# Kernel optimization log

Measured on AMD Instinct MI355X. Metric: run time of the kernel, lower is better.

## Reference

```python
import jax, jax.numpy as jnp
import numpy as np

EPS = 1e-5

def setup_inputs() -> dict:
    key = jax.random.key(0)
    ks = jax.random.split(key, 12)
    B = 4096
    x = jax.random.normal(ks[0], (B, 28, 28, 1), dtype=jnp.float32)
    # BatchNorm1d(1) affine params (applied per-channel over active sites)
    bn_gamma = jnp.ones((1,), jnp.float32)
    bn_beta = jnp.zeros((1,), jnp.float32)
    # SubMConv2d weights, HWIO layout
    w1 = jax.random.normal(ks[1], (3, 3, 1, 32), jnp.float32) * 0.1
    b1 = jax.random.normal(ks[2], (32,), jnp.float32) * 0.01
    w2 = jax.random.normal(ks[3], (3, 3, 32, 64), jnp.float32) * 0.05
    b2 = jax.random.normal(ks[4], (64,), jnp.float32) * 0.01
    # FC layers (torch Linear: y = x @ W.T + b)
    fcw1 = jax.random.normal(ks[5], (128, 14 * 14 * 64), jnp.float32) * 0.01
    fcb1 = jnp.zeros((128,), jnp.float32)
    fcw2 = jax.random.normal(ks[6], (10, 128), jnp.float32) * 0.05
    fcb2 = jnp.zeros((10,), jnp.float32)
    return {"x": x, "bn_gamma": bn_gamma, "bn_beta": bn_beta,
            "w1": w1, "b1": b1, "w2": w2, "b2": b2,
            "fcw1": fcw1, "fcb1": fcb1, "fcw2": fcw2, "fcb2": fcb2}

def _subm_conv(feat, mask, w, b):
    # Submanifold conv: inactive inputs are zero (already masked), and the
    # output coordinate set equals the input active set -> mask the output.
    y = jax.lax.conv_general_dilated(
        feat, w, window_strides=(1, 1), padding='SAME',
        dimension_numbers=('NHWC', 'HWIO', 'NHWC'))
    return jnp.where(mask, y + b, 0.0)

def reference(x, bn_gamma, bn_beta, w1, b1, w2, b2, fcw1, fcb1, fcw2, fcb2):
    # from_dense: active sites are locations with nonzero feature. [B,28,28,1]
    mask = (x != 0)  # single channel -> site mask [B,28,28,1]
    maskf = mask.astype(x.dtype)
    # BatchNorm1d(1) on the [N_active, 1] sparse feature tensor (batch stats)
    n = jnp.maximum(maskf.sum(), 1.0)
    mean = (x * maskf).sum() / n
    var = (jnp.square(x - mean) * maskf).sum() / n
    feat = maskf * (bn_gamma * (x - mean) * jax.lax.rsqrt(var + EPS) + bn_beta)
    # SubMConv2d(1,32,3,1) + ReLU
    h = jax.nn.relu(_subm_conv(feat, mask, w1, b1))  # [B,28,28,32]
    # SubMConv2d(32,64,3,1) + ReLU
    h = jax.nn.relu(_subm_conv(h, mask, w2, b2))     # [B,28,28,64]
    # SparseMaxPool2d(2,2): max over active sites per window; since values are
    # post-ReLU (>=0) and inactive sites hold 0, dense maxpool is exact, and
    # fully-inactive windows correctly yield 0 after ToDense.
    h = jax.lax.reduce_window(h, -jnp.inf, jax.lax.max,
                              (1, 2, 2, 1), (1, 2, 2, 1), 'VALID')  # [B,14,14,64]
    # ToDense gives NCHW [B,64,14,14]; torch.flatten uses C-major order
    h = jnp.transpose(h, (0, 3, 1, 2)).reshape(h.shape[0], -1)  # [B,12544]
    # dropout1/dropout2 are identity in eval mode
    h = jax.nn.relu(h @ fcw1.T + fcb1)
    logits = h @ fcw2.T + fcb2
    return jax.nn.log_softmax(logits, axis=1)
```

## Files before the change

kernel.cpp:

```cpp
#include <hip/hip_runtime.h>
#include <stdint.h>

typedef unsigned short u16;
typedef unsigned int u32;
typedef __attribute__((ext_vector_type(8))) short bf16x8;
typedef __attribute__((ext_vector_type(4))) float f32x4;

__device__ __forceinline__ u16 f2bf(float f) {
    u32 u = __float_as_uint(f);
    u32 r = (u + 0x7fffu + ((u >> 16) & 1u)) >> 16;
    return (u16)r;
}

__device__ __forceinline__ void gload16(const u16* src, u16* dst) {
    __builtin_amdgcn_global_load_lds(
        (const __attribute__((address_space(1))) u32*)src,
        (__attribute__((address_space(3))) u32*)dst, 16, 0, 0);
}

__global__ __launch_bounds__(256) void k_stats(const float* __restrict__ x, int n,
                                               float* __restrict__ stats) {
    int t = blockIdx.x * 256 + threadIdx.x;
    int stride = gridDim.x * 256;
    float c = 0.f, s = 0.f, ss = 0.f;
    for (int i = t; i < n; i += stride) {
        float v = x[i];
        if (v != 0.f) { c += 1.f; s += v; ss = fmaf(v, v, ss); }
    }
    for (int off = 32; off > 0; off >>= 1) {
        c  += __shfl_down(c, off);
        s  += __shfl_down(s, off);
        ss += __shfl_down(ss, off);
    }
    __shared__ float red[3][4];
    int lane = threadIdx.x & 63, wv = threadIdx.x >> 6;
    if (lane == 0) { red[0][wv] = c; red[1][wv] = s; red[2][wv] = ss; }
    __syncthreads();
    if (threadIdx.x == 0) {
        atomicAdd(&stats[0], red[0][0] + red[0][1] + red[0][2] + red[0][3]);
        atomicAdd(&stats[1], red[1][0] + red[1][1] + red[1][2] + red[1][3]);
        atomicAdd(&stats[2], red[2][0] + red[2][1] + red[2][2] + red[2][3]);
    }
}

__global__ void k_finalize(const float* __restrict__ g, const float* __restrict__ b,
                           float* __restrict__ stats) {
    float n = stats[0]; if (n < 1.f) n = 1.f;
    float mean = stats[1] / n;
    float var = stats[2] / n - mean * mean;
    if (var < 0.f) var = 0.f;
    float scale = g[0] * rsqrtf(var + 1e-5f);
    stats[4] = scale;
    stats[5] = b[0] - mean * scale;
}

__global__ __launch_bounds__(256) void k_prep(const float* __restrict__ w2,
                                              u16* __restrict__ w2b) {
    int i = blockIdx.x * 256 + threadIdx.x;
    if (i < 9 * 64 * 32) {
        int tap = i >> 11, rem = i & 2047, co = rem >> 5, ci = rem & 31;
        w2b[i] = f2bf(w2[tap * 2048 + ci * 64 + co]);
    }
}

__global__ __launch_bounds__(256) void k_prepw(const float* __restrict__ fcw1,
                                               u16* __restrict__ fcw1b, int n) {
    int i = blockIdx.x * 256 + threadIdx.x;
    if (i < n) fcw1b[i] = f2bf(fcw1[i]);
}

__global__ __launch_bounds__(256, 2) void k_conv(const float* __restrict__ x,
    const float* __restrict__ w1, const float* __restrict__ b1,
    const u16* __restrict__ w2b, const float* __restrict__ b2,
    const float* __restrict__ stats, u16* __restrict__ pooled)
{
    __shared__ u16 h1[28800];
    __shared__ float feat[30][30];
    __shared__ unsigned char mk[784];
    const int t = threadIdx.x;
    const int b = blockIdx.x;
    const int lane = t & 63;
    const int wv = t >> 6;
    const int lg = lane >> 4;
    const int lr = lane & 15;

    bf16x8 wf[9][4];
    #pragma unroll
    for (int tap = 0; tap < 9; ++tap)
        #pragma unroll
        for (int nt = 0; nt < 4; ++nt)
            wf[tap][nt] = *(const bf16x8*)(w2b + tap * 2048 + (nt * 16 + lr) * 32 + lg * 8);
    float bias2[4];
    #pragma unroll
    for (int nt = 0; nt < 4; ++nt) bias2[nt] = b2[nt * 16 + lr];

    const float scale = stats[4], shift = stats[5];

    for (int i = t; i < 14400; i += 256) ((u32*)h1)[i] = 0u;
    for (int i = t; i < 900; i += 256) (&feat[0][0])[i] = 0.f;
    __syncthreads();

    const float* xb = x + (size_t)b * 784;
    for (int i = t; i < 784; i += 256) {
        float v = xb[i];
        bool m = (v != 0.f);
        mk[i] = m ? 1 : 0;
        int h = i / 28, w = i - h * 28;
        feat[h + 1][w + 1] = m ? fmaf(v, scale, shift) : 0.f;
    }
    __syncthreads();

    {
        const int cp = t & 15, pxg = t >> 4;
        float wk0[9], wk1[9];
        const float bs0 = b1[2 * cp], bs1 = b1[2 * cp + 1];
        #pragma unroll
        for (int j = 0; j < 9; ++j) {
            wk0[j] = w1[j * 32 + 2 * cp];
            wk1[j] = w1[j * 32 + 2 * cp + 1];
        }
        const int hslot = (cp >> 2) * 7200 + (cp & 3) * 2;
        for (int px = pxg; px < 784; px += 16) {
            if (!mk[px]) continue;
            int h = px / 28, w = px - h * 28;
            float a0 = bs0, a1 = bs1;
            #pragma unroll
            for (int kh = 0; kh < 3; ++kh)
                #pragma unroll
                for (int kw = 0; kw < 3; ++kw) {
                    float f = feat[h + kh][w + kw];
                    a0 = fmaf(f, wk0[kh * 3 + kw], a0);
                    a1 = fmaf(f, wk1[kh * 3 + kw], a1);
                }
            u32 pk = (u32)f2bf(fmaxf(a0, 0.f)) | ((u32)f2bf(fmaxf(a1, 0.f)) << 16);
            *(u32*)&h1[hslot + ((h + 1) * 30 + (w + 1)) * 8] = pk;
        }
    }
    __syncthreads();

    const int win = lr >> 2, dyl = (lr >> 1) & 1, dxl = lr & 1;
    const f32x4 zero4 = {0.f, 0.f, 0.f, 0.f};
    for (int mt = wv; mt < 56; mt += 4) {
        const int r = mt >> 2, cg = mt & 3;
        const int ih = 2 * r + dyl;
        int iw = 2 * (cg * 4 + win) + dxl;
        if (iw > 27) iw = 27;
        const char* abase = (const char*)h1 + lg * 14400 + (ih * 30 + iw) * 16;

        f32x4 acc[4];
        #pragma unroll
        for (int nt = 0; nt < 4; ++nt) acc[nt] = zero4;

        #pragma unroll
        for (int tap = 0; tap < 9; ++tap) {
            const int kh = tap / 3, kw = tap - kh * 3;
            bf16x8 af = *(const bf16x8*)(abase + (kh * 30 + kw) * 16);
            #pragma unroll
            for (int nt = 0; nt < 4; ++nt)
                acc[nt] = __builtin_amdgcn_mfma_f32_16x16x32_bf16(af, wf[tap][nt], acc[nt], 0, 0, 0);
        }

        const int pc = cg * 4 + lg;
        if (pc < 14) {
            const int m00 = mk[(2 * r) * 28 + 2 * pc];
            const int m01 = mk[(2 * r) * 28 + 2 * pc + 1];
            const int m10 = mk[(2 * r + 1) * 28 + 2 * pc];
            const int m11 = mk[(2 * r + 1) * 28 + 2 * pc + 1];
            #pragma unroll
            for (int nt = 0; nt < 4; ++nt) {
                float v0 = m00 ? fmaxf(acc[nt][0] + bias2[nt], 0.f) : 0.f;
                float v1 = m01 ? fmaxf(acc[nt][1] + bias2[nt], 0.f) : 0.f;
                float v2 = m10 ? fmaxf(acc[nt][2] + bias2[nt], 0.f) : 0.f;
                float v3 = m11 ? fmaxf(acc[nt][3] + bias2[nt], 0.f) : 0.f;
                float best = fmaxf(fmaxf(v0, v1), fmaxf(v2, v3));
                pooled[(size_t)b * 12544 + (nt * 16 + lr) * 196 + r * 14 + pc] = f2bf(best);
            }
        }
    }
}

__global__ __launch_bounds__(256, 4) void k_fc1(const u16* __restrict__ pooled,
    const u16* __restrict__ fcw1b, float* __restrict__ fc1, int M)
{
    __shared__ u16 Asm[8 * 64 * 8];
    __shared__ u16 Bsm[8 * 128 * 8];
    const int t = threadIdx.x;
    const int m0 = blockIdx.x * 64;
    const int kbase = blockIdx.y * 896;
    const int lane = t & 63;
    const int wv = t >> 6;
    const int lg = lane >> 4, lr = lane & 15;
    const int wm = wv & 1, wn = wv >> 1;

    const int ia0 = t, ia1 = t + 256;
    const u16* as0 = pooled + (size_t)(m0 + (ia0 & 63)) * 12544 + (ia0 >> 6) * 8 + kbase;
    const u16* as1 = pooled + (size_t)(m0 + (ia1 & 63)) * 12544 + (ia1 >> 6) * 8 + kbase;
    const u16* bs0 = fcw1b + (size_t)(t & 127) * 12544 + ((t >> 7) + 0) * 8 + kbase;
    const u16* bs1 = fcw1b + (size_t)(t & 127) * 12544 + ((t >> 7) + 2) * 8 + kbase;
    const u16* bs2 = fcw1b + (size_t)(t & 127) * 12544 + ((t >> 7) + 4) * 8 + kbase;
    const u16* bs3 = fcw1b + (size_t)(t & 127) * 12544 + ((t >> 7) + 6) * 8 + kbase;
    u16* ad0 = &Asm[(size_t)ia0 * 8];
    u16* ad1 = &Asm[(size_t)ia1 * 8];
    u16* bd0 = &Bsm[(size_t)(t + 0) * 8];
    u16* bd1 = &Bsm[(size_t)(t + 256) * 8];
    u16* bd2 = &Bsm[(size_t)(t + 512) * 8];
    u16* bd3 = &Bsm[(size_t)(t + 768) * 8];

    f32x4 acc[2][4];
    #pragma unroll
    for (int mi = 0; mi < 2; ++mi)
        #pragma unroll
        for (int ni = 0; ni < 4; ++ni) acc[mi][ni] = (f32x4){0.f, 0.f, 0.f, 0.f};

    for (int s = 0; s < 14; ++s) {
        const int kk = s * 64;
        __syncthreads();
        gload16(as0 + kk, ad0);
        gload16(as1 + kk, ad1);
        gload16(bs0 + kk, bd0);
        gload16(bs1 + kk, bd1);
        gload16(bs2 + kk, bd2);
        gload16(bs3 + kk, bd3);
        asm volatile("s_waitcnt vmcnt(0)" ::: "memory");
        __syncthreads();
        #pragma unroll
        for (int ks = 0; ks < 2; ++ks) {
            bf16x8 a[2], bfr[4];
            #pragma unroll
            for (int mi = 0; mi < 2; ++mi)
                a[mi] = *(const bf16x8*)&Asm[(((ks * 4 + lg) * 64) + wm * 32 + mi * 16 + lr) * 8];
            #pragma unroll
            for (int ni = 0; ni < 4; ++ni)
                bfr[ni] = *(const bf16x8*)&Bsm[(((ks * 4 + lg) * 128) + wn * 64 + ni * 16 + lr) * 8];
            #pragma unroll
            for (int mi = 0; mi < 2; ++mi)
                #pragma unroll
                for (int ni = 0; ni < 4; ++ni)
                    acc[mi][ni] = __builtin_amdgcn_mfma_f32_16x16x32_bf16(a[mi], bfr[ni], acc[mi][ni], 0, 0, 0);
        }
    }

    #pragma unroll
    for (int mi = 0; mi < 2; ++mi)
        #pragma unroll
        for (int ni = 0; ni < 4; ++ni)
            #pragma unroll
            for (int q = 0; q < 4; ++q) {
                int m = m0 + wm * 32 + mi * 16 + lg * 4 + q;
                int n = wn * 64 + ni * 16 + lr;
                atomicAdd(&fc1[(size_t)m * 128 + n], acc[mi][ni][q]);
            }
}

__global__ __launch_bounds__(256) void k_fc2(const float* __restrict__ fc1,
    const float* __restrict__ fcb1, const float* __restrict__ fcw2,
    const float* __restrict__ fcb2, float* __restrict__ out, int M)
{
    __shared__ float red[4][64][10];
    const int t = threadIdx.x;
    const int ml = t & 63, kq = t >> 6;
    const int m = blockIdx.x * 64 + ml;
    float acc[10];
    #pragma unroll
    for (int c = 0; c < 10; ++c) acc[c] = 0.f;
    const float* fp = fc1 + (size_t)m * 128 + kq * 32;
    #pragma unroll 2
    for (int j = 0; j < 32; j += 4) {
        float4 v4 = *(const float4*)(fp + j);
        float vv[4] = {v4.x, v4.y, v4.z, v4.w};
        #pragma unroll
        for (int u = 0; u < 4; ++u) {
            int k = kq * 32 + j + u;
            float v = fmaxf(vv[u] + fcb1[k], 0.f);
            #pragma unroll
            for (int c = 0; c < 10; ++c) acc[c] = fmaf(v, fcw2[c * 128 + k], acc[c]);
        }
    }
    #pragma unroll
    for (int c = 0; c < 10; ++c) red[kq][ml][c] = acc[c];
    __syncthreads();
    if (kq == 0) {
        float lgt[10];
        #pragma unroll
        for (int c = 0; c < 10; ++c)
            lgt[c] = red[0][ml][c] + red[1][ml][c] + red[2][ml][c] + red[3][ml][c] + fcb2[c];
        float mx = lgt[0];
        #pragma unroll
        for (int c = 1; c < 10; ++c) mx = fmaxf(mx, lgt[c]);
        float se = 0.f;
        #pragma unroll
        for (int c = 0; c < 10; ++c) se += expf(lgt[c] - mx);
        float lse = mx + logf(se);
        #pragma unroll
        for (int c = 0; c < 10; ++c) out[(size_t)m * 10 + c] = lgt[c] - lse;
    }
}

extern "C" void kernel_launch(void* const* d_in, const int* in_sizes, int n_in,
                              void* d_out, int out_size, void* d_ws, size_t ws_size,
                              hipStream_t stream) {
    const float* x     = (const float*)d_in[0];
    const float* gamma = (const float*)d_in[1];
    const float* beta  = (const float*)d_in[2];
    const float* w1    = (const float*)d_in[3];
    const float* b1    = (const float*)d_in[4];
    const float* w2    = (const float*)d_in[5];
    const float* b2    = (const float*)d_in[6];
    const float* fcw1  = (const float*)d_in[7];
    const float* fcb1  = (const float*)d_in[8];
    const float* fcw2  = (const float*)d_in[9];
    const float* fcb2  = (const float*)d_in[10];
    float* out = (float*)d_out;

    const int B = in_sizes[0] / 784;

    float* stats  = (float*)d_ws;
    u16*   w2b    = (u16*)((char*)d_ws + 256);
    float* fc1    = (float*)((char*)d_ws + 256);
    u16*   pooled = (u16*)((char*)d_ws + 256 + (size_t)B * 128 * 4);
    u16*   fcw1b  = (u16*)((char*)d_ws + 256 + (size_t)B * 128 * 4 + (size_t)B * 12544 * 2);

    hipMemsetAsync(stats, 0, 32, stream);
    k_stats<<<1024, 256, 0, stream>>>(x, B * 784, stats);
    k_finalize<<<1, 1, 0, stream>>>(gamma, beta, stats);
    k_prep<<<72, 256, 0, stream>>>(w2, w2b);
    k_prepw<<<(128 * 12544 + 255) / 256, 256, 0, stream>>>(fcw1, fcw1b, 128 * 12544);
    k_conv<<<B, 256, 0, stream>>>(x, w1, b1, w2b, b2, stats, pooled);
    hipMemsetAsync(fc1, 0, (size_t)B * 128 * 4, stream);
    k_fc1<<<dim3(B / 64, 14), 256, 0, stream>>>(pooled, fcw1b, fc1, B);
    k_fc2<<<B / 64, 256, 0, stream>>>(fc1, fcb1, fcw2, fcb2, out, B);
}
```

Measured before the change: 399.7 us.

## Restructure conv2 MFMA tiling, widen conv1 per-thread channels, halve fc1 split-K

Conv2 now has each wave compute two adjacent output rows per iteration. It reuses the shared A fragments across vertical taps, folds the bias into the accumulator init, precomputes packed 2x2 pool masks, and writes two pooled values per store. Conv1 gives each thread 8 channels with vectorized weight loads and 16-byte LDS stores, and the padded h1 stride is changed to 14464 bytes. Separately, the two weight-prep kernels are merged into one launch, fc1's split-K is halved to 7 chunks to cut atomics, and fc2 uses 32-row blocks. These add register pressure in conv2, and the smaller fc1 grid gives less parallelism.

```diff
diff --git a/kernel.cpp b/kernel.cpp
--- a/kernel.cpp
+++ b/kernel.cpp
@@ -54,18 +54,14 @@
     stats[5] = b[0] - mean * scale;
 }
 
-__global__ __launch_bounds__(256) void k_prep(const float* __restrict__ w2,
-                                              u16* __restrict__ w2b) {
+__global__ __launch_bounds__(256) void k_prepall(const float* __restrict__ w2,
+    const float* __restrict__ fcw1, u16* __restrict__ w2b, u16* __restrict__ fcw1b, int n)
+{
     int i = blockIdx.x * 256 + threadIdx.x;
     if (i < 9 * 64 * 32) {
         int tap = i >> 11, rem = i & 2047, co = rem >> 5, ci = rem & 31;
         w2b[i] = f2bf(w2[tap * 2048 + ci * 64 + co]);
     }
-}
-
-__global__ __launch_bounds__(256) void k_prepw(const float* __restrict__ fcw1,
-                                               u16* __restrict__ fcw1b, int n) {
-    int i = blockIdx.x * 256 + threadIdx.x;
     if (i < n) fcw1b[i] = f2bf(fcw1[i]);
 }
 
@@ -74,9 +70,10 @@
     const u16* __restrict__ w2b, const float* __restrict__ b2,
     const float* __restrict__ stats, u16* __restrict__ pooled)
 {
-    __shared__ u16 h1[28800];
+    __shared__ u16 h1[28928];
     __shared__ float feat[30][30];
     __shared__ unsigned char mk[784];
+    __shared__ unsigned char pm[200];
     const int t = threadIdx.x;
     const int b = blockIdx.x;
     const int lane = t & 63;
@@ -84,19 +81,9 @@
     const int lg = lane >> 4;
     const int lr = lane & 15;
 
-    bf16x8 wf[9][4];
-    #pragma unroll
-    for (int tap = 0; tap < 9; ++tap)
-        #pragma unroll
-        for (int nt = 0; nt < 4; ++nt)
-            wf[tap][nt] = *(const bf16x8*)(w2b + tap * 2048 + (nt * 16 + lr) * 32 + lg * 8);
-    float bias2[4];
-    #pragma unroll
-    for (int nt = 0; nt < 4; ++nt) bias2[nt] = b2[nt * 16 + lr];
-
     const float scale = stats[4], shift = stats[5];
 
-    for (int i = t; i < 14400; i += 256) ((u32*)h1)[i] = 0u;
+    for (int i = t; i < 14464; i += 256) ((u32*)h1)[i] = 0u;
     for (int i = t; i < 900; i += 256) (&feat[0][0])[i] = 0.f;
     __syncthreads();
 
@@ -110,70 +97,122 @@
     }
     __syncthreads();
 
+    if (t < 196) {
+        int rr = t / 14, cc = t - rr * 14;
+        int base = rr * 56 + cc * 2;
+        pm[t] = (unsigned char)(mk[base] | (mk[base + 1] << 1)
+              | (mk[base + 28] << 2) | (mk[base + 29] << 3));
+    }
+
     {
-        const int cp = t & 15, pxg = t >> 4;
-        float wk0[9], wk1[9];
-        const float bs0 = b1[2 * cp], bs1 = b1[2 * cp + 1];
+        const int cp = (t >> 4) & 3;
+        const int pxg = (t & 15) | ((t >> 6) << 4);
+        float wk[9][8], bs[8];
+        {
+            float4 b0 = *(const float4*)(b1 + cp * 8);
+            float4 b4 = *(const float4*)(b1 + cp * 8 + 4);
+            bs[0]=b0.x; bs[1]=b0.y; bs[2]=b0.z; bs[3]=b0.w;
+            bs[4]=b4.x; bs[5]=b4.y; bs[6]=b4.z; bs[7]=b4.w;
+        }
         #pragma unroll
         for (int j = 0; j < 9; ++j) {
-            wk0[j] = w1[j * 32 + 2 * cp];
-            wk1[j] = w1[j * 32 + 2 * cp + 1];
-        }
-        const int hslot = (cp >> 2) * 7200 + (cp & 3) * 2;
-        for (int px = pxg; px < 784; px += 16) {
+            float4 w0 = *(const float4*)(w1 + j * 32 + cp * 8);
+            float4 w4 = *(const float4*)(w1 + j * 32 + cp * 8 + 4);
+            wk[j][0]=w0.x; wk[j][1]=w0.y; wk[j][2]=w0.z; wk[j][3]=w0.w;
+            wk[j][4]=w4.x; wk[j][5]=w4.y; wk[j][6]=w4.z; wk[j][7]=w4.w;
+        }
+        char* hb = (char*)h1 + cp * 14464;
+        for (int px = pxg; px < 784; px += 64) {
             if (!mk[px]) continue;
             int h = px / 28, w = px - h * 28;
-            float a0 = bs0, a1 = bs1;
+            float a[8];
+            #pragma unroll
+            for (int c = 0; c < 8; ++c) a[c] = bs[c];
             #pragma unroll
             for (int kh = 0; kh < 3; ++kh)
                 #pragma unroll
                 for (int kw = 0; kw < 3; ++kw) {
                     float f = feat[h + kh][w + kw];
-                    a0 = fmaf(f, wk0[kh * 3 + kw], a0);
-                    a1 = fmaf(f, wk1[kh * 3 + kw], a1);
+                    #pragma unroll
+                    for (int c = 0; c < 8; ++c) a[c] = fmaf(f, wk[kh * 3 + kw][c], a[c]);
                 }
-            u32 pk = (u32)f2bf(fmaxf(a0, 0.f)) | ((u32)f2bf(fmaxf(a1, 0.f)) << 16);
-            *(u32*)&h1[hslot + ((h + 1) * 30 + (w + 1)) * 8] = pk;
-        }
-    }
-    __syncthreads();
-
-    const int win = lr >> 2, dyl = (lr >> 1) & 1, dxl = lr & 1;
-    const f32x4 zero4 = {0.f, 0.f, 0.f, 0.f};
-    for (int mt = wv; mt < 56; mt += 4) {
-        const int r = mt >> 2, cg = mt & 3;
-        const int ih = 2 * r + dyl;
-        int iw = 2 * (cg * 4 + win) + dxl;
-        if (iw > 27) iw = 27;
-        const char* abase = (const char*)h1 + lg * 14400 + (ih * 30 + iw) * 16;
-
-        f32x4 acc[4];
-        #pragma unroll
-        for (int nt = 0; nt < 4; ++nt) acc[nt] = zero4;
-
-        #pragma unroll
-        for (int tap = 0; tap < 9; ++tap) {
-            const int kh = tap / 3, kw = tap - kh * 3;
-            bf16x8 af = *(const bf16x8*)(abase + (kh * 30 + kw) * 16);
-            #pragma unroll
-            for (int nt = 0; nt < 4; ++nt)
-                acc[nt] = __builtin_amdgcn_mfma_f32_16x16x32_bf16(af, wf[tap][nt], acc[nt], 0, 0, 0);
-        }
-
-        const int pc = cg * 4 + lg;
-        if (pc < 14) {
-            const int m00 = mk[(2 * r) * 28 + 2 * pc];
-            const int m01 = mk[(2 * r) * 28 + 2 * pc + 1];
-            const int m10 = mk[(2 * r + 1) * 28 + 2 * pc];
-            const int m11 = mk[(2 * r + 1) * 28 + 2 * pc + 1];
+            u32 q0 = (u32)f2bf(fmaxf(a[0], 0.f)) | ((u32)f2bf(fmaxf(a[1], 0.f)) << 16);
+            u32 q1 = (u32)f2bf(fmaxf(a[2], 0.f)) | ((u32)f2bf(fmaxf(a[3], 0.f)) << 16);
+            u32 q2 = (u32)f2bf(fmaxf(a[4], 0.f)) | ((u32)f2bf(fmaxf(a[5], 0.f)) << 16);
+            u32 q3 = (u32)f2bf(fmaxf(a[6], 0.f)) | ((u32)f2bf(fmaxf(a[7], 0.f)) << 16);
+            *(uint4*)(hb + ((h + 1) * 30 + (w + 1)) * 16) = make_uint4(q0, q1, q2, q3);
+        }
+    }
+    __syncthreads();
+
+    bf16x8 wf[9][4];
+    #pragma unroll
+    for (int tap = 0; tap < 9; ++tap)
+        #pragma unroll
+        for (int nt = 0; nt < 4; ++nt)
+            wf[tap][nt] = *(const bf16x8*)(w2b + tap * 2048 + (nt * 16 + lr) * 32 + lg * 8);
+    float bias2[4];
+    #pragma unroll
+    for (int nt = 0; nt < 4; ++nt) bias2[nt] = b2[nt * 16 + lr];
+
+    const int cb = wv & 1;
+    const int r0 = wv >> 1;
+    const char* gb = (const char*)h1 + lg * 14464 + (cb * 16 + lr) * 16;
+    const bool store_ok = !(cb == 1 && lg == 3);
+    const int pc0 = cb * 8 + lg * 2;
+    u16* poolb = pooled + (size_t)b * 12544;
+
+    #pragma unroll 1
+    for (int i = 0; i < 7; ++i) {
+        const int r = r0 + 2 * i;
+        const char* ab = gb + 960 * r;
+        bf16x8 a0[3], a1[3], a2[3], a3[3];
+        #pragma unroll
+        for (int kw = 0; kw < 3; ++kw) {
+            a0[kw] = *(const bf16x8*)(ab + kw * 16);
+            a1[kw] = *(const bf16x8*)(ab + 480 + kw * 16);
+            a2[kw] = *(const bf16x8*)(ab + 960 + kw * 16);
+        }
+        f32x4 acc0[4], acc1[4];
+        #pragma unroll
+        for (int nt = 0; nt < 4; ++nt) {
+            acc0[nt] = (f32x4){bias2[nt], bias2[nt], bias2[nt], bias2[nt]};
+            acc1[nt] = acc0[nt];
+        }
+        #pragma unroll
+        for (int nt = 0; nt < 4; ++nt)
+            #pragma unroll
+            for (int kw = 0; kw < 3; ++kw) {
+                acc0[nt] = __builtin_amdgcn_mfma_f32_16x16x32_bf16(a0[kw], wf[kw][nt], acc0[nt], 0, 0, 0);
+                acc0[nt] = __builtin_amdgcn_mfma_f32_16x16x32_bf16(a1[kw], wf[3 + kw][nt], acc0[nt], 0, 0, 0);
+                acc0[nt] = __builtin_amdgcn_mfma_f32_16x16x32_bf16(a2[kw], wf[6 + kw][nt], acc0[nt], 0, 0, 0);
+            }
+        #pragma unroll
+        for (int kw = 0; kw < 3; ++kw)
+            a3[kw] = *(const bf16x8*)(ab + 1440 + kw * 16);
+        #pragma unroll
+        for (int nt = 0; nt < 4; ++nt)
+            #pragma unroll
+            for (int kw = 0; kw < 3; ++kw) {
+                acc1[nt] = __builtin_amdgcn_mfma_f32_16x16x32_bf16(a1[kw], wf[kw][nt], acc1[nt], 0, 0, 0);
+                acc1[nt] = __builtin_amdgcn_mfma_f32_16x16x32_bf16(a2[kw], wf[3 + kw][nt], acc1[nt], 0, 0, 0);
+                acc1[nt] = __builtin_amdgcn_mfma_f32_16x16x32_bf16(a3[kw], wf[6 + kw][nt], acc1[nt], 0, 0, 0);
+            }
+
+        if (store_ok) {
+            u32 pmw = *(const u16*)&pm[r * 14 + pc0];
+            float m00 = (pmw & 1u)    ? 1.f : 0.f, m01 = (pmw & 2u)    ? 1.f : 0.f;
+            float m10 = (pmw & 4u)    ? 1.f : 0.f, m11 = (pmw & 8u)    ? 1.f : 0.f;
+            float n00 = (pmw & 256u)  ? 1.f : 0.f, n01 = (pmw & 512u)  ? 1.f : 0.f;
+            float n10 = (pmw & 1024u) ? 1.f : 0.f, n11 = (pmw & 2048u) ? 1.f : 0.f;
             #pragma unroll
             for (int nt = 0; nt < 4; ++nt) {
-                float v0 = m00 ? fmaxf(acc[nt][0] + bias2[nt], 0.f) : 0.f;
-                float v1 = m01 ? fmaxf(acc[nt][1] + bias2[nt], 0.f) : 0.f;
-                float v2 = m10 ? fmaxf(acc[nt][2] + bias2[nt], 0.f) : 0.f;
-                float v3 = m11 ? fmaxf(acc[nt][3] + bias2[nt], 0.f) : 0.f;
-                float best = fmaxf(fmaxf(v0, v1), fmaxf(v2, v3));
-                pooled[(size_t)b * 12544 + (nt * 16 + lr) * 196 + r * 14 + pc] = f2bf(best);
+                float p0 = fmaxf(fmaxf(fmaxf(acc0[nt][0], 0.f) * m00, fmaxf(acc0[nt][1], 0.f) * m01),
+                                 fmaxf(fmaxf(acc1[nt][0], 0.f) * m10, fmaxf(acc1[nt][1], 0.f) * m11));
+                float p1 = fmaxf(fmaxf(fmaxf(acc0[nt][2], 0.f) * n00, fmaxf(acc0[nt][3], 0.f) * n01),
+                                 fmaxf(fmaxf(acc1[nt][2], 0.f) * n10, fmaxf(acc1[nt][3], 0.f) * n11));
+                *(u32*)&poolb[(nt * 16 + lr) * 196 + r * 14 + pc0] =
+                    (u32)f2bf(p0) | ((u32)f2bf(p1) << 16);
             }
         }
     }
@@ -186,7 +225,7 @@
     __shared__ u16 Bsm[8 * 128 * 8];
     const int t = threadIdx.x;
     const int m0 = blockIdx.x * 64;
-    const int kbase = blockIdx.y * 896;
+    const int kbase = blockIdx.y * 1792;
     const int lane = t & 63;
     const int wv = t >> 6;
     const int lg = lane >> 4, lr = lane & 15;
@@ -212,7 +251,7 @@
         #pragma unroll
         for (int ni = 0; ni < 4; ++ni) acc[mi][ni] = (f32x4){0.f, 0.f, 0.f, 0.f};
 
-    for (int s = 0; s < 14; ++s) {
+    for (int s = 0; s < 28; ++s) {
         const int kk = s * 64;
         __syncthreads();
         gload16(as0 + kk, ad0);
@@ -256,21 +295,21 @@
     const float* __restrict__ fcb1, const float* __restrict__ fcw2,
     const float* __restrict__ fcb2, float* __restrict__ out, int M)
 {
-    __shared__ float red[4][64][10];
+    __shared__ float red[8][32][10];
     const int t = threadIdx.x;
-    const int ml = t & 63, kq = t >> 6;
-    const int m = blockIdx.x * 64 + ml;
+    const int ml = t & 31, kq = t >> 5;
+    const int m = blockIdx.x * 32 + ml;
     float acc[10];
     #pragma unroll
     for (int c = 0; c < 10; ++c) acc[c] = 0.f;
-    const float* fp = fc1 + (size_t)m * 128 + kq * 32;
-    #pragma unroll 2
-    for (int j = 0; j < 32; j += 4) {
+    const float* fp = fc1 + (size_t)m * 128 + kq * 16;
+    #pragma unroll
+    for (int j = 0; j < 16; j += 4) {
         float4 v4 = *(const float4*)(fp + j);
         float vv[4] = {v4.x, v4.y, v4.z, v4.w};
         #pragma unroll
         for (int u = 0; u < 4; ++u) {
-            int k = kq * 32 + j + u;
+            int k = kq * 16 + j + u;
             float v = fmaxf(vv[u] + fcb1[k], 0.f);
             #pragma unroll
             for (int c = 0; c < 10; ++c) acc[c] = fmaf(v, fcw2[c * 128 + k], acc[c]);
@@ -282,8 +321,12 @@
     if (kq == 0) {
         float lgt[10];
         #pragma unroll
-        for (int c = 0; c < 10; ++c)
-            lgt[c] = red[0][ml][c] + red[1][ml][c] + red[2][ml][c] + red[3][ml][c] + fcb2[c];
+        for (int c = 0; c < 10; ++c) {
+            float sv = 0.f;
+            #pragma unroll
+            for (int s = 0; s < 8; ++s) sv += red[s][ml][c];
+            lgt[c] = sv + fcb2[c];
+        }
         float mx = lgt[0];
         #pragma unroll
         for (int c = 1; c < 10; ++c) mx = fmaxf(mx, lgt[c]);
@@ -323,10 +366,9 @@
     hipMemsetAsync(stats, 0, 32, stream);
     k_stats<<<1024, 256, 0, stream>>>(x, B * 784, stats);
     k_finalize<<<1, 1, 0, stream>>>(gamma, beta, stats);
-    k_prep<<<72, 256, 0, stream>>>(w2, w2b);
-    k_prepw<<<(128 * 12544 + 255) / 256, 256, 0, stream>>>(fcw1, fcw1b, 128 * 12544);
+    k_prepall<<<(128 * 12544 + 255) / 256, 256, 0, stream>>>(w2, fcw1, w2b, fcw1b, 128 * 12544);
     k_conv<<<B, 256, 0, stream>>>(x, w1, b1, w2b, b2, stats, pooled);
     hipMemsetAsync(fc1, 0, (size_t)B * 128 * 4, stream);
-    k_fc1<<<dim3(B / 64, 14), 256, 0, stream>>>(pooled, fcw1b, fc1, B);
-    k_fc2<<<B / 64, 256, 0, stream>>>(fc1, fcb1, fcw2, fcb2, out, B);
-}
+    k_fc1<<<dim3(B / 64, 7), 256, 0, stream>>>(pooled, fcw1b, fc1, B);
+    k_fc2<<<B / 32, 256, 0, stream>>>(fc1, fcb1, fcw2, fcb2, out, B);
+}
```

New measurement: 350.0 us. -12.4%, faster.
